# Performance work log

Measured on AMD Instinct MI355X. Metric: run time of the kernel, lower is better.

## Reference

```python
import jax, jax.numpy as jnp
import numpy as np

B, N, D_MODEL, H, D_FF, NB_FEAT = 2, 2048, 512, 8, 2048, 256
DH = D_MODEL // H


def layer_norm(x, g, b, eps=1e-5):
    mu = jnp.mean(x, axis=-1, keepdims=True)
    var = jnp.mean((x - mu) ** 2, axis=-1, keepdims=True)
    return g * (x - mu) / jnp.sqrt(var + eps) + b


def softmax_kernel(data, proj, is_query, eps=1e-4):
    # Performer FAVOR+ positive random features. data: [b,h,n,dh], proj: [m,dh]
    dn = data.shape[-1] ** -0.25
    ratio = proj.shape[0] ** -0.5
    dd = jnp.einsum('bhnd,jd->bhnj', dn * data, proj)
    diag = (jnp.sum(data ** 2, axis=-1, keepdims=True) * 0.5) * (dn ** 2)
    if is_query:
        m = jnp.max(dd, axis=-1, keepdims=True)
    else:
        m = jnp.max(dd)
    return ratio * (jnp.exp(dd - diag - m) + eps)


def setup_inputs() -> dict:
    key = jax.random.key(0)
    ks = jax.random.split(key, 12)
    sd = D_MODEL ** -0.5
    sf = D_FF ** -0.5
    return {
        'x': jax.random.normal(ks[0], (B, N, D_MODEL), jnp.float32),
        'Wq': jax.random.normal(ks[1], (D_MODEL, D_MODEL), jnp.float32) * sd,
        'bq': jnp.zeros((D_MODEL,), jnp.float32),
        'Wk': jax.random.normal(ks[2], (D_MODEL, D_MODEL), jnp.float32) * sd,
        'bk': jnp.zeros((D_MODEL,), jnp.float32),
        'Wv': jax.random.normal(ks[3], (D_MODEL, D_MODEL), jnp.float32) * sd,
        'bv': jnp.zeros((D_MODEL,), jnp.float32),
        'Wo': jax.random.normal(ks[4], (D_MODEL, D_MODEL), jnp.float32) * sd,
        'bo': jnp.zeros((D_MODEL,), jnp.float32),
        'proj': jax.random.normal(ks[5], (NB_FEAT, DH), jnp.float32),
        'W1': jax.random.normal(ks[6], (D_MODEL, D_FF), jnp.float32) * sd,
        'b1': jnp.zeros((D_FF,), jnp.float32),
        'W2': jax.random.normal(ks[7], (D_FF, D_MODEL), jnp.float32) * sf,
        'b2': jnp.zeros((D_MODEL,), jnp.float32),
        'g1': jnp.ones((D_MODEL,), jnp.float32),
        'beta1': jnp.zeros((D_MODEL,), jnp.float32),
        'g2': jnp.ones((D_MODEL,), jnp.float32),
        'beta2': jnp.zeros((D_MODEL,), jnp.float32),
    }


def reference(x, Wq, bq, Wk, bk, Wv, bv, Wo, bo, proj, W1, b1, W2, b2, g1, beta1, g2, beta2):
    b, n, d = x.shape
    heads = lambda W, bias: (x @ W + bias).reshape(b, n, H, DH).transpose(0, 2, 1, 3)  # bhnd
    q = softmax_kernel(heads(Wq, bq), proj, is_query=True)   # [b,h,n,m]
    k = softmax_kernel(heads(Wk, bk), proj, is_query=False)  # [b,h,n,m]
    v = heads(Wv, bv)                                        # [b,h,n,dh]
    # non-causal linear attention
    k_sum = jnp.sum(k, axis=-2)                                   # [b,h,m]
    D_inv = 1.0 / jnp.einsum('bhnf,bhf->bhn', q, k_sum)           # [b,h,n]
    context = jnp.einsum('bhnf,bhne->bhfe', k, v)                 # [b,h,m,dh]
    out = jnp.einsum('bhfe,bhnf,bhn->bhne', context, q, D_inv)    # [b,h,n,dh]
    # output_attentions=True: effective attention matrix (abs, head-mean, detached)
    attn = jnp.einsum('bhnf,bhmf->bhnm', q, k) * D_inv[..., None]
    attn_weight = jax.lax.stop_gradient(jnp.mean(jnp.abs(attn), axis=1))  # [b,n,n]
    out = out.transpose(0, 2, 1, 3).reshape(b, n, d)
    out = out @ Wo + bo
    # NOTE: original module has no residual connections
    h1 = layer_norm(out, g1, beta1)
    ff = jax.nn.relu(h1 @ W1 + b1) @ W2 + b2
    y = layer_norm(ff, g2, beta2)
    return y, attn_weight
```

## Files before the change

kernel.cpp:

```cpp
#include <hip/hip_runtime.h>
#include <math.h>

#define B_SZ   2
#define N_TOK  2048
#define DM     512
#define NH     8
#define DHH    64
#define NF     256
#define DFF    2048
#define HF     2048
#define LDQKV  1536

constexpr float DN_SCALE   = 0.35355339059327373f;
constexpr float DIAG_SCALE = 0.0625f;
constexpr float RATIO      = 0.0625f;
constexpr float FEPS       = 1e-4f;
constexpr float LN_EPS     = 1e-5f;

typedef __attribute__((ext_vector_type(8))) short bf16x8;
typedef __attribute__((ext_vector_type(8))) _Float16 f16x8;
typedef __attribute__((ext_vector_type(4))) float f32x4;

__device__ __forceinline__ short f2b(float f) {
  union { float f; unsigned u; } x; x.f = f;
  unsigned r = (x.u + 0x7fff + ((x.u >> 16) & 1)) >> 16;
  return (short)r;
}
__device__ __forceinline__ float b2f(short s) {
  union { unsigned u; float f; } x; x.u = ((unsigned)(unsigned short)s) << 16;
  return x.f;
}
__device__ __forceinline__ void gload16(const void* g, void* l) {
  __builtin_amdgcn_global_load_lds((const __attribute__((address_space(1))) void*)g,
                                   (__attribute__((address_space(3))) void*)l, 16, 0, 0);
}
__device__ __forceinline__ int swz64(int row, int kbyte) {
  return (row * 128 + kbyte) ^ ((row & 7) << 4);
}
__device__ __forceinline__ float reduce_bmax512(const float* __restrict__ bmax,
                                                float* __restrict__ red) {
  int t = threadIdx.x;
  float m = fmaxf(bmax[t], bmax[t + 256]);
  #pragma unroll
  for (int o = 1; o < 64; o <<= 1) m = fmaxf(m, __shfl_xor(m, o, 64));
  if ((t & 63) == 0) red[t >> 6] = m;
  __syncthreads();
  float r = fmaxf(fmaxf(red[0], red[1]), fmaxf(red[2], red[3]));
  __syncthreads();
  return r;
}

constexpr size_t OFF_CTXP  = 0;
constexpr size_t OFF_QB    = 4194304;
constexpr size_t OFF_OUT2  = 0;
constexpr size_t OFF_FF2   = 0;
constexpr size_t OFF_QFB   = 8388608;
constexpr size_t OFF_KB    = 12582912;
constexpr size_t OFF_QKV   = 16777216;
constexpr size_t OFF_FF1B  = 16777216;
constexpr size_t OFF_AOB   = 20971520;
constexpr size_t OFF_H1B   = 22020096;
constexpr size_t OFF_WOT   = 23068672;
constexpr size_t OFF_W1T   = 23199744;
constexpr size_t OFF_W2T   = 23724032;
constexpr size_t OFF_KSUM  = 24248320;
constexpr size_t OFF_DINV  = 24252416;
constexpr size_t OFF_CTXT  = 24285184;
constexpr size_t OFF_BMAX  = 24416256;
constexpr size_t OFF_ROWC  = 24416832;
constexpr size_t OFF_PART  = 24420928;
constexpr size_t OFF_VSUMP = 24552000;


template<bool RELU, bool OUT_BF16, bool BIAS>
__device__ __forceinline__ void gemm128_tile(short* As, short* Bs, int bx, int by,
                                             const short* __restrict__ A,
                                             const short* __restrict__ Bt,
                                             const float* __restrict__ bias,
                                             void* __restrict__ Cout, int K, int ldC) {
  int tid = threadIdx.x, lane = tid & 63, wave = tid >> 6;
  int wm = wave >> 1, wn = wave & 1;
  int bm = by * 128, bn = bx * 128;
  int srow = tid >> 3, scol = (tid & 7) * 8;
  f32x4 acc[4][4] = {};
  for (int k0 = 0; k0 < K; k0 += 64) {
    #pragma unroll
    for (int c = 0; c < 4; ++c) {
      int r = c * 32 + srow;
      gload16(A + (size_t)(bm + r) * K + k0 + scol, As + c * 2048 + wave * 512);
      gload16(Bt + (size_t)(bn + r) * K + k0 + scol, Bs + c * 2048 + wave * 512);
    }
    __syncthreads();
    #pragma unroll
    for (int kk = 0; kk < 2; ++kk) {
      bf16x8 af[4], bf[4];
      int kq = kk * 32 + (lane >> 4) * 8;
      #pragma unroll
      for (int i = 0; i < 4; ++i)
        af[i] = *(const bf16x8*)&As[(wm * 64 + i * 16 + (lane & 15)) * 64 + kq];
      #pragma unroll
      for (int j = 0; j < 4; ++j)
        bf[j] = *(const bf16x8*)&Bs[(wn * 64 + j * 16 + (lane & 15)) * 64 + kq];
      #pragma unroll
      for (int i = 0; i < 4; ++i)
        #pragma unroll
        for (int j = 0; j < 4; ++j)
          acc[i][j] = __builtin_amdgcn_mfma_f32_16x16x32_bf16(af[i], bf[j], acc[i][j], 0, 0, 0);
    }
    __syncthreads();
  }
  int row0 = bm + wm * 64, col0 = bn + wn * 64;
  #pragma unroll
  for (int i = 0; i < 4; ++i) {
    #pragma unroll
    for (int j = 0; j < 4; ++j) {
      int col = col0 + j * 16 + (lane & 15);
      float bv = BIAS ? bias[col] : 0.f;
      #pragma unroll
      for (int r = 0; r < 4; ++r) {
        int row = row0 + i * 16 + (lane >> 4) * 4 + r;
        float v = acc[i][j][r] + bv;
        if (RELU) v = fmaxf(v, 0.f);
        size_t off = (size_t)row * ldC + col;
        if (OUT_BF16) ((short*)Cout)[off] = f2b(v);
        else          ((float*)Cout)[off] = v;
      }
    }
  }
}

template<bool RELU, bool OUT_BF16>
__device__ __forceinline__ void bn64_tile(short* As, short* Bs, int bn, int bm,
                                          const short* __restrict__ A,
                                          const short* __restrict__ Bt,
                                          const float* __restrict__ bias,
                                          void* __restrict__ Cout, int N, int K) {
  int tid = threadIdx.x, lane = tid & 63, wave = tid >> 6;
  int srow = tid >> 3, scol = (tid & 7) * 8;
  f32x4 acc[2][4] = {};
  for (int k0 = 0; k0 < K; k0 += 64) {
    #pragma unroll
    for (int c = 0; c < 4; ++c)
      gload16(A + (size_t)(bm + c * 32 + srow) * K + k0 + scol, As + c * 2048 + wave * 512);
    #pragma unroll
    for (int c = 0; c < 2; ++c)
      gload16(Bt + (size_t)(bn + c * 32 + srow) * K + k0 + scol, Bs + c * 2048 + wave * 512);
    __syncthreads();
    #pragma unroll
    for (int kk = 0; kk < 2; ++kk) {
      bf16x8 af[2], bf[4];
      int kq = kk * 32 + (lane >> 4) * 8;
      #pragma unroll
      for (int i = 0; i < 2; ++i)
        af[i] = *(const bf16x8*)&As[(wave * 32 + i * 16 + (lane & 15)) * 64 + kq];
      #pragma unroll
      for (int j = 0; j < 4; ++j)
        bf[j] = *(const bf16x8*)&Bs[(j * 16 + (lane & 15)) * 64 + kq];
      #pragma unroll
      for (int i = 0; i < 2; ++i)
        #pragma unroll
        for (int j = 0; j < 4; ++j)
          acc[i][j] = __builtin_amdgcn_mfma_f32_16x16x32_bf16(af[i], bf[j], acc[i][j], 0, 0, 0);
    }
    __syncthreads();
  }
  #pragma unroll
  for (int i = 0; i < 2; ++i) {
    #pragma unroll
    for (int j = 0; j < 4; ++j) {
      int col = bn + j * 16 + (lane & 15);
      float bv = bias[col];
      #pragma unroll
      for (int r = 0; r < 4; ++r) {
        int row = bm + wave * 32 + i * 16 + (lane >> 4) * 4 + r;
        float v = acc[i][j][r] + bv;
        if (RELU) v = fmaxf(v, 0.f);
        if (OUT_BF16) ((short*)Cout)[(size_t)row * N + col] = f2b(v);
        else          ((float*)Cout)[(size_t)row * N + col] = v;
      }
    }
  }
}

__device__ __forceinline__ void pv_tile(short* As, short* Bs, int pid,
                                        const short* __restrict__ qfb,
                                        const short* __restrict__ ctxT,
                                        const float* __restrict__ Dinv,
                                        short* __restrict__ aob) {
  int tid = threadIdx.x, lane = tid & 63, wave = tid >> 6;
  int srow = tid >> 3, scol = (tid & 7) * 8;
  int bx = pid & 15, bh = pid >> 4;
  int b = bh >> 3, h = bh & 7;
  int n0 = bx * 128;

  f32x4 acc[2][4] = {};
  for (int k0 = 0; k0 < NF; k0 += 64) {
    #pragma unroll
    for (int c = 0; c < 4; ++c) {
      int r = c * 32 + srow;
      gload16(qfb + (size_t)(b * N_TOK + n0 + r) * HF + h * NF + k0 + scol,
              As + c * 2048 + wave * 512);
    }
    #pragma unroll
    for (int c = 0; c < 2; ++c) {
      int r = c * 32 + srow;
      gload16(ctxT + (size_t)bh * 16384 + (size_t)r * 256 + k0 + scol,
              Bs + c * 2048 + wave * 512);
    }
    __syncthreads();
    #pragma unroll
    for (int kk = 0; kk < 2; ++kk) {
      bf16x8 af[2], bf[4];
      int kq = kk * 32 + (lane >> 4) * 8;
      #pragma unroll
      for (int i = 0; i < 2; ++i)
        af[i] = *(const bf16x8*)&As[(wave * 32 + i * 16 + (lane & 15)) * 64 + kq];
      #pragma unroll
      for (int j = 0; j < 4; ++j)
        bf[j] = *(const bf16x8*)&Bs[(j * 16 + (lane & 15)) * 64 + kq];
      #pragma unroll
      for (int i = 0; i < 2; ++i)
        #pragma unroll
        for (int j = 0; j < 4; ++j)
          acc[i][j] = __builtin_amdgcn_mfma_f32_16x16x32_bf16(af[i], bf[j], acc[i][j], 0, 0, 0);
    }
    __syncthreads();
  }
  #pragma unroll
  for (int i = 0; i < 2; ++i) {
    #pragma unroll
    for (int j = 0; j < 4; ++j) {
      int e = j * 16 + (lane & 15);
      #pragma unroll
      for (int r = 0; r < 4; ++r) {
        int n = n0 + wave * 32 + i * 16 + (lane >> 4) * 4 + r;
        float dv = Dinv[bh * N_TOK + n];
        aob[(size_t)(b * N_TOK + n) * DM + h * DHH + e] = f2b(acc[i][j][r] * dv);
      }
    }
  }
}


__global__ __launch_bounds__(256)
void gemm_mfma_qkv(const short* __restrict__ A, const short* __restrict__ Bt,
                   float* __restrict__ Cout) {
  __shared__ short As[128 * 64];
  __shared__ short Bs[128 * 64];
  gemm128_tile<false, false, false>(As, Bs, blockIdx.x, blockIdx.y, A, Bt, nullptr,
                                    Cout, DM, LDQKV);
}

__global__ __launch_bounds__(256)
void pv_kernel(const short* __restrict__ qfb, const short* __restrict__ ctxT,
               const float* __restrict__ Dinv, short* __restrict__ aob) {
  __shared__ short As[128 * 64];
  __shared__ short Bs[64 * 64];
  pv_tile(As, Bs, blockIdx.x, qfb, ctxT, Dinv, aob);
}

__global__ __launch_bounds__(256)
void gemm_bn64_wo(const short* __restrict__ A, const short* __restrict__ Bt,
                  const float* __restrict__ bias, float* __restrict__ Cout) {
  __shared__ short As[128 * 64];
  __shared__ short Bs[64 * 64];
  bn64_tile<false, false>(As, Bs, blockIdx.x * 64, blockIdx.y * 128, A, Bt, bias, Cout, DM, DM);
}

template<bool RELU, bool OUT_BF16>
__global__ __launch_bounds__(256)
void gemm_bn64(const short* __restrict__ A, const short* __restrict__ Bt,
               const float* __restrict__ bias, void* __restrict__ Cout,
               int M, int N, int K) {
  __shared__ short As[128 * 64];
  __shared__ short Bs[64 * 64];
  bn64_tile<RELU, OUT_BF16>(As, Bs, blockIdx.x * 64, blockIdx.y * 128, A, Bt, bias, Cout, N, K);
}

__global__ __launch_bounds__(256)
void fatC1_kernel(const short* __restrict__ qb, const short* __restrict__ kb,
                  const float* __restrict__ rowc, float* __restrict__ attnw,
                  const short* __restrict__ h1b, const short* __restrict__ W1t,
                  const float* __restrict__ b1, short* __restrict__ ff1b) {
  __shared__ short As[2][128 * 64];
  __shared__ short Bs[2][128 * 64];
  int bid = blockIdx.x;
  int tid = threadIdx.x, lane = tid & 63, wave = tid >> 6;
  int srow = tid >> 3, scol = (tid & 7) * 8;

  if (bid < 512) {
    int z = bid >> 8, flat = bid & 255;
    int tile = flat >> 4, wi = flat & 15;
    int by = (tile >> 2) * 4 + (wi >> 2);
    int bx = (tile & 3) * 4 + (wi & 3);
    int bm = by * 128, bn = bx * 128;
    const short* Ab = qb + (size_t)z * N_TOK * HF;
    const short* Bb = kb + (size_t)z * N_TOK * HF;
    const float* rc = rowc + (size_t)z * N_TOK;
    float* out = attnw + (size_t)z * N_TOK * N_TOK;
    int wm = wave >> 1, wn = wave & 1;
    f32x4 acc[4][4] = {};

    #pragma unroll
    for (int c = 0; c < 4; ++c) {
      int r = c * 32 + srow;
      gload16(Ab + (size_t)(bm + r) * HF + scol, As[0] + c * 2048 + wave * 512);
      gload16(Bb + (size_t)(bn + r) * HF + scol, Bs[0] + c * 2048 + wave * 512);
    }
    for (int it = 0; it < HF / 64; ++it) {
      int cur = it & 1;
      if (it + 1 < HF / 64) {
        int k1 = (it + 1) * 64;
        short* An = As[cur ^ 1];
        short* Bn = Bs[cur ^ 1];
        #pragma unroll
        for (int c = 0; c < 4; ++c) {
          int r = c * 32 + srow;
          gload16(Ab + (size_t)(bm + r) * HF + k1 + scol, An + c * 2048 + wave * 512);
          gload16(Bb + (size_t)(bn + r) * HF + k1 + scol, Bn + c * 2048 + wave * 512);
        }
        asm volatile("s_waitcnt vmcnt(8)" ::: "memory");
      } else {
        asm volatile("s_waitcnt vmcnt(0)" ::: "memory");
      }
      __builtin_amdgcn_s_barrier();
      __builtin_amdgcn_sched_barrier(0);
      const short* Ac = As[cur];
      const short* Bc = Bs[cur];
      #pragma unroll
      for (int kk = 0; kk < 2; ++kk) {
        bf16x8 af[4], bf[4];
        int kq = kk * 32 + (lane >> 4) * 8;
        #pragma unroll
        for (int i = 0; i < 4; ++i)
          af[i] = *(const bf16x8*)&Ac[(wm * 64 + i * 16 + (lane & 15)) * 64 + kq];
        #pragma unroll
        for (int j = 0; j < 4; ++j)
          bf[j] = *(const bf16x8*)&Bc[(wn * 64 + j * 16 + (lane & 15)) * 64 + kq];
        #pragma unroll
        for (int i = 0; i < 4; ++i)
          #pragma unroll
          for (int j = 0; j < 4; ++j)
            acc[i][j] = __builtin_amdgcn_mfma_f32_16x16x32_bf16(af[i], bf[j], acc[i][j], 0, 0, 0);
      }
      __builtin_amdgcn_sched_barrier(0);
      __builtin_amdgcn_s_barrier();
    }
    int row0 = bm + wm * 64, col0 = bn + wn * 64;
    #pragma unroll
    for (int i = 0; i < 4; ++i) {
      #pragma unroll
      for (int j = 0; j < 4; ++j) {
        int col = col0 + j * 16 + (lane & 15);
        #pragma unroll
        for (int r = 0; r < 4; ++r) {
          int row = row0 + i * 16 + (lane >> 4) * 4 + r;
          out[(size_t)row * N_TOK + col] = acc[i][j][r] + rc[row];
        }
      }
    }
  } else {
    int flat = bid - 512;
    gemm128_tile<true, true, true>(As[0], Bs[0], flat & 15, flat >> 4, h1b, W1t, b1, ff1b,
                                   DM, DFF);
  }
}

__global__ void prep_kernel(const float* __restrict__ x, short* __restrict__ xb,
                            const float* Wq, const float* Wk, const float* Wv, const float* Wo,
                            short* Wqt, short* Wkt, short* Wvt, short* Wot,
                            const float* W1, short* W1t, const float* W2, short* W2t) {
  __shared__ float t[64][65];
  int id = blockIdx.x, tid = threadIdx.x;
  if (id >= 768) {
    size_t base = ((size_t)(id - 768) * 256 + tid) * 8;
    #pragma unroll
    for (int u = 0; u < 8; ++u) xb[base + u] = f2b(x[base + u]);
    return;
  }
  const float* W; short* Wt; int K, N, bx, by;
  if (id < 256) {
    int z = id >> 6, sub = id & 63;
    W  = (z == 0) ? Wq : (z == 1) ? Wk : (z == 2) ? Wv : Wo;
    Wt = (z == 0) ? Wqt : (z == 1) ? Wkt : (z == 2) ? Wvt : Wot;
    K = 512; N = 512; bx = sub & 7; by = sub >> 3;
  } else if (id < 512) {
    int sub = id - 256;
    W = W1; Wt = W1t; K = 512; N = 2048; bx = sub & 31; by = sub >> 5;
  } else {
    int sub = id - 512;
    W = W2; Wt = W2t; K = 2048; N = 512; bx = sub & 7; by = sub >> 3;
  }
  int k0 = by * 64, n0 = bx * 64;
  int lx = tid & 63, ly = tid >> 6;
  for (int r = ly; r < 64; r += 4)
    t[r][lx] = W[(size_t)(k0 + r) * N + n0 + lx];
  __syncthreads();
  for (int r = ly; r < 64; r += 4)
    Wt[(size_t)(n0 + r) * K + k0 + lx] = f2b(t[lx][r]);
}

__global__ __launch_bounds__(256)
void feat_mfma_kernel(const float* __restrict__ qkv, const float* __restrict__ bq,
                      const float* __restrict__ bk, const float* __restrict__ proj,
                      short* __restrict__ qfb, short* __restrict__ kbo,
                      float* __restrict__ part, float* __restrict__ bmax) {
  __shared__ short qh[64 * 64], ql[64 * 64];
  __shared__ short ph[128 * 64], pl[128 * 64];
  __shared__ float dpart[64][4];
  __shared__ float diag[64];
  __shared__ float wred[4];
  __shared__ float colp[4][256];
  int t = threadIdx.x;
  bool isq = (blockIdx.z == 0);
  int coff = isq ? 0 : 512;
  const float* bias = isq ? bq : bk;
  short* qout = isq ? qfb : kbo;
  int bh = blockIdx.y, b = bh >> 3, h = bh & 7;
  int n0 = blockIdx.x * 64;
  int lane = t & 63, w = t >> 6, l15 = lane & 15, lq = lane >> 4;

  {
    int r = t >> 2, cg = (t & 3) * 16;
    const float* src = qkv + (size_t)(b * N_TOK + n0 + r) * LDQKV + coff + h * 64 + cg;
    const float* bs = bias + h * 64 + cg;
    float ss = 0.f;
    #pragma unroll
    for (int c2 = 0; c2 < 2; ++c2) {
      f16x8 H, L;
      #pragma unroll
      for (int u = 0; u < 8; ++u) {
        float xv = src[c2 * 8 + u] + bs[c2 * 8 + u];
        ss += xv * xv;
        _Float16 hi = (_Float16)xv;
        H[u] = hi;
        L[u] = (_Float16)(xv - (float)hi);
      }
      int off = swz64(r, cg * 2 + c2 * 16);
      *(f16x8*)((char*)qh + off) = H;
      *(f16x8*)((char*)ql + off) = L;
    }
    dpart[r][t & 3] = ss;
  }
  __syncthreads();
  if (t < 64)
    diag[t] = (dpart[t][0] + dpart[t][1] + dpart[t][2] + dpart[t][3]) * DIAG_SCALE;

  f16x8 ah[2], al[2];
  #pragma unroll
  for (int kk = 0; kk < 2; ++kk) {
    int off = swz64(w * 16 + l15, kk * 64 + lq * 16);
    ah[kk] = *(f16x8*)((char*)qh + off);
    al[kk] = *(f16x8*)((char*)ql + off);
  }

  f32x4 acc[16] = {};
  #pragma unroll
  for (int half = 0; half < 2; ++half) {
    __syncthreads();
    {
      int r = t & 127, cg = (t >> 7) * 32;
      const float* src = proj + (size_t)(half * 128 + r) * DHH + cg;
      #pragma unroll
      for (int c2 = 0; c2 < 4; ++c2) {
        f16x8 H, L;
        #pragma unroll
        for (int u = 0; u < 8; ++u) {
          float xv = src[c2 * 8 + u];
          _Float16 hi = (_Float16)xv;
          H[u] = hi;
          L[u] = (_Float16)(xv - (float)hi);
        }
        int off = swz64(r, cg * 2 + c2 * 16);
        *(f16x8*)((char*)ph + off) = H;
        *(f16x8*)((char*)pl + off) = L;
      }
    }
    __syncthreads();
    #pragma unroll
    for (int jl = 0; jl < 8; ++jl) {
      int row = jl * 16 + l15;
      #pragma unroll
      for (int kk = 0; kk < 2; ++kk) {
        int off = swz64(row, kk * 64 + lq * 16);
        f16x8 bh8 = *(f16x8*)((char*)ph + off);
        f16x8 bl8 = *(f16x8*)((char*)pl + off);
        acc[half * 8 + jl] = __builtin_amdgcn_mfma_f32_16x16x32_f16(ah[kk], bh8, acc[half * 8 + jl], 0, 0, 0);
        acc[half * 8 + jl] = __builtin_amdgcn_mfma_f32_16x16x32_f16(al[kk], bh8, acc[half * 8 + jl], 0, 0, 0);
        acc[half * 8 + jl] = __builtin_amdgcn_mfma_f32_16x16x32_f16(ah[kk], bl8, acc[half * 8 + jl], 0, 0, 0);
      }
    }
  }

  if (isq) {
    #pragma unroll
    for (int r = 0; r < 4; ++r) {
      float mx = -3.4e38f;
      #pragma unroll
      for (int j = 0; j < 16; ++j) mx = fmaxf(mx, acc[j][r]);
      #pragma unroll
      for (int o = 1; o < 16; o <<= 1) mx = fmaxf(mx, __shfl_xor(mx, o, 64));
      int lrow = w * 16 + lq * 4 + r;
      float dg = diag[lrow];
      float ddm = mx * DN_SCALE;
      size_t base = (size_t)(b * N_TOK + n0 + lrow) * HF + h * NF + l15;
      #pragma unroll
      for (int j = 0; j < 16; ++j) {
        float v = RATIO * (expf(acc[j][r] * DN_SCALE - dg - ddm) + FEPS);
        qout[base + j * 16] = f2b(v);
      }
    }
  } else {
    float mxall = -3.4e38f;
    float cs[16];
    #pragma unroll
    for (int j = 0; j < 16; ++j) cs[j] = 0.f;
    #pragma unroll
    for (int r = 0; r < 4; ++r) {
      int lrow = w * 16 + lq * 4 + r;
      float dg = diag[lrow];
      size_t base = (size_t)(b * N_TOK + n0 + lrow) * HF + h * NF + l15;
      #pragma unroll
      for (int j = 0; j < 16; ++j) {
        float a = acc[j][r];
        mxall = fmaxf(mxall, a);
        float e = expf(a * DN_SCALE - dg);
        cs[j] += e;
        qout[base + j * 16] = f2b(e);
      }
    }
    #pragma unroll
    for (int j = 0; j < 16; ++j) {
      cs[j] += __shfl_xor(cs[j], 16, 64);
      cs[j] += __shfl_xor(cs[j], 32, 64);
    }
    if (lq == 0) {
      #pragma unroll
      for (int j = 0; j < 16; ++j) colp[w][j * 16 + l15] = cs[j];
    }
    #pragma unroll
    for (int o = 1; o < 64; o <<= 1) mxall = fmaxf(mxall, __shfl_xor(mxall, o, 64));
    if (lane == 0) wred[w] = mxall;
    __syncthreads();
    part[(size_t)(bh * 32 + blockIdx.x) * 256 + t] =
        colp[0][t] + colp[1][t] + colp[2][t] + colp[3][t];
    if (t == 0)
      bmax[bh * 32 + blockIdx.x] =
          fmaxf(fmaxf(wred[0], wred[1]), fmaxf(wred[2], wred[3])) * DN_SCALE;
  }
}

__global__ __launch_bounds__(256)
void ctx_part_kernel(const short* __restrict__ kb, const float* __restrict__ qkv,
                     const float* __restrict__ bv, float* __restrict__ ctxp,
                     float* __restrict__ vsump) {
  int bh = blockIdx.y, b = bh >> 3, h = bh & 7;
  int ns = blockIdx.z * 128;
  int tid = threadIdx.x;
  if (blockIdx.x == 4) {
    __shared__ float vred[4][64];
    int e = tid & 63, q = tid >> 6;
    float s = 0.f;
    for (int nn = q * 32; nn < q * 32 + 32; ++nn)
      s += qkv[(size_t)(b * N_TOK + ns + nn) * LDQKV + 1024 + h * DHH + e];
    vred[q][e] = s;
    __syncthreads();
    if (tid < 64)
      vsump[((size_t)blockIdx.z * 16 + bh) * 64 + tid] =
          vred[0][tid] + vred[1][tid] + vred[2][tid] + vred[3][tid] + 128.f * bv[h * DHH + tid];
    return;
  }
  int f0 = blockIdx.x * 64;
  __shared__ float kf[32][68];
  __shared__ float vs[32][68];
  int tf = (tid >> 4) * 4, te = (tid & 15) * 4;
  int nn8 = tid >> 3, f8 = (tid & 7) * 8;
  float bvv[8];
  #pragma unroll
  for (int u = 0; u < 8; ++u) bvv[u] = bv[h * DHH + f8 + u];
  float acc[4][4] = {};
  for (int n0 = ns; n0 < ns + 128; n0 += 32) {
    bf16x8 kv8 = *(const bf16x8*)&kb[(size_t)(b * N_TOK + n0 + nn8) * HF + h * NF + f0 + f8];
    #pragma unroll
    for (int u = 0; u < 8; ++u) kf[nn8][f8 + u] = b2f(kv8[u]);
    const float* vrow = qkv + (size_t)(b * N_TOK + n0 + nn8) * LDQKV + 1024 + h * DHH + f8;
    #pragma unroll
    for (int u = 0; u < 8; ++u) vs[nn8][f8 + u] = vrow[u] + bvv[u];
    __syncthreads();
    #pragma unroll
    for (int nn = 0; nn < 32; nn++) {
      float a[4], bb[4];
      #pragma unroll
      for (int i = 0; i < 4; i++) a[i] = kf[nn][tf + i];
      #pragma unroll
      for (int j = 0; j < 4; j++) bb[j] = vs[nn][te + j];
      #pragma unroll
      for (int i = 0; i < 4; i++)
        #pragma unroll
        for (int j = 0; j < 4; j++) acc[i][j] += a[i] * bb[j];
    }
    __syncthreads();
  }
  #pragma unroll
  for (int i = 0; i < 4; i++)
    #pragma unroll
    for (int j = 0; j < 4; j++)
      ctxp[(size_t)blockIdx.z * 262144 + (size_t)bh * 16384 +
           (size_t)(f0 + tf + i) * 64 + te + j] = acc[i][j];
}

__global__ __launch_bounds__(256)
void smallfat_kernel(const float* __restrict__ part, const float* __restrict__ bmax,
                     float* __restrict__ ksum, const float* __restrict__ ctxp,
                     const float* __restrict__ vsump, short* __restrict__ ctxT) {
  __shared__ float T[64][65];
  __shared__ float red[4];
  int t = threadIdx.x;
  float m = reduce_bmax512(bmax, red);
  float s = expf(-m);
  if (blockIdx.x < 16) {
    int bh = blockIdx.x;
    float sum = 0.f;
    #pragma unroll 8
    for (int c = 0; c < 32; ++c) sum += part[(size_t)(bh * 32 + c) * 256 + t];
    ksum[bh * 256 + t] = RATIO * (s * sum + (float)N_TOK * FEPS);
  } else {
    int id = blockIdx.x - 16;
    int ftile = id & 3, bh = id >> 2;
    int e = t & 63, q = t >> 6;
    float vsum_e = 0.f;
    #pragma unroll
    for (int c = 0; c < 16; ++c) vsum_e += vsump[((size_t)c * 16 + bh) * 64 + e];
    #pragma unroll
    for (int i = 0; i < 16; ++i) {
      int fl = i * 4 + q;
      size_t idx = (size_t)bh * 16384 + (size_t)(ftile * 64 + fl) * 64 + e;
      float sum = 0.f;
      #pragma unroll
      for (int c = 0; c < 16; ++c) sum += ctxp[(size_t)c * 262144 + idx];
      T[fl][e] = RATIO * (s * sum + FEPS * vsum_e);
    }
    __syncthreads();
    #pragma unroll
    for (int i = 0; i < 16; ++i) {
      int er = i * 4 + q;
      ctxT[(size_t)bh * 16384 + (size_t)er * 256 + ftile * 64 + e] = f2b(T[e][er]);
    }
  }
}

__global__ __launch_bounds__(256)
void dinvqs_kernel(const short* __restrict__ qfb, const float* __restrict__ ksum,
                   const float* __restrict__ bmax, float* __restrict__ Dinv,
                   float* __restrict__ rowc, short* __restrict__ qb) {
  __shared__ float red[4];
  __shared__ float wsum[4];
  int R = blockIdx.x;
  int b = R >> 11, n = R & 2047;
  int t = threadIdx.x;
  float m = reduce_bmax512(bmax, red);
  float sc = RATIO * expf(-m);
  bf16x8 qv = *(const bf16x8*)(qfb + (size_t)R * HF + t * 8);
  const float* ks = ksum + b * 2048 + t * 8;
  float p = 0.f;
  #pragma unroll
  for (int u = 0; u < 8; ++u) p += b2f(qv[u]) * ks[u];
  #pragma unroll
  for (int o = 1; o < 32; o <<= 1) p += __shfl_xor(p, o, 64);
  float d = 1.0f / p;
  if ((t & 31) == 0) Dinv[(b * NH + (t >> 5)) * N_TOK + n] = d;
  float dv = d * 0.125f;
  float qs = 0.f;
  bf16x8 o8;
  #pragma unroll
  for (int u = 0; u < 8; ++u) {
    float qb_f = b2f(qv[u]) * dv;
    qs += qb_f;
    o8[u] = f2b(qb_f * sc);
  }
  *(bf16x8*)(qb + (size_t)R * HF + t * 8) = o8;
  #pragma unroll
  for (int o = 1; o < 64; o <<= 1) qs += __shfl_xor(qs, o, 64);
  if ((t & 63) == 0) wsum[t >> 6] = qs;
  __syncthreads();
  if (t == 0) rowc[R] = RATIO * FEPS * (wsum[0] + wsum[1] + wsum[2] + wsum[3]);
}

template<bool OUT_BF16>
__global__ void ln_kernel(const float* __restrict__ x, const float* __restrict__ g,
                          const float* __restrict__ beta, void* __restrict__ y) {
  int row = blockIdx.x, t = threadIdx.x;
  __shared__ float red[4];
  __shared__ float bcast[2];
  const float* xr = x + (size_t)row * DM;
  float v0 = xr[t], v1 = xr[t + 256];
  float s = v0 + v1;
  #pragma unroll
  for (int o = 32; o > 0; o >>= 1) s += __shfl_xor(s, o, 64);
  if ((t & 63) == 0) red[t >> 6] = s;
  __syncthreads();
  if (t == 0) bcast[0] = (red[0] + red[1] + red[2] + red[3]) * (1.0f / 512.0f);
  __syncthreads();
  float mean = bcast[0];
  float d0 = v0 - mean, d1 = v1 - mean;
  float s2 = d0 * d0 + d1 * d1;
  #pragma unroll
  for (int o = 32; o > 0; o >>= 1) s2 += __shfl_xor(s2, o, 64);
  if ((t & 63) == 0) red[t >> 6] = s2;
  __syncthreads();
  if (t == 0) bcast[1] = (red[0] + red[1] + red[2] + red[3]) * (1.0f / 512.0f);
  __syncthreads();
  float inv = rsqrtf(bcast[1] + LN_EPS);
  float o0 = g[t] * d0 * inv + beta[t];
  float o1 = g[t + 256] * d1 * inv + beta[t + 256];
  if (OUT_BF16) {
    ((short*)y)[(size_t)row * DM + t] = f2b(o0);
    ((short*)y)[(size_t)row * DM + t + 256] = f2b(o1);
  } else {
    ((float*)y)[(size_t)row * DM + t] = o0;
    ((float*)y)[(size_t)row * DM + t + 256] = o1;
  }
}

extern "C" void kernel_launch(void* const* d_in, const int* in_sizes, int n_in,
                              void* d_out, int out_size, void* d_ws, size_t ws_size,
                              hipStream_t stream) {
  const float* x     = (const float*)d_in[0];
  const float* Wq    = (const float*)d_in[1];
  const float* bq    = (const float*)d_in[2];
  const float* Wk    = (const float*)d_in[3];
  const float* bk    = (const float*)d_in[4];
  const float* Wv    = (const float*)d_in[5];
  const float* bv    = (const float*)d_in[6];
  const float* Wo    = (const float*)d_in[7];
  const float* bo    = (const float*)d_in[8];
  const float* proj  = (const float*)d_in[9];
  const float* W1    = (const float*)d_in[10];
  const float* b1    = (const float*)d_in[11];
  const float* W2    = (const float*)d_in[12];
  const float* b2    = (const float*)d_in[13];
  const float* g1    = (const float*)d_in[14];
  const float* beta1 = (const float*)d_in[15];
  const float* g2    = (const float*)d_in[16];
  const float* beta2 = (const float*)d_in[17];

  float* ws = (float*)d_ws;
  float* y_out = (float*)d_out;
  float* attnw = y_out + (size_t)B_SZ * N_TOK * DM;

  float* ctxp  = ws + OFF_CTXP;
  short* qb    = (short*)(ws + OFF_QB);
  float* out2  = ws + OFF_OUT2;
  float* ff2   = ws + OFF_FF2;
  short* ff1b  = (short*)(ws + OFF_FF1B);
  short* qfb   = (short*)(ws + OFF_QFB);
  short* xb    = (short*)(ws + OFF_QFB);
  short* kb    = (short*)(ws + OFF_KB);
  short* Wqkvt = (short*)(ws + OFF_KB);
  float* QKVlin = ws + OFF_QKV;
  short* aob   = (short*)(ws + OFF_AOB);
  short* h1b   = (short*)(ws + OFF_H1B);
  short* Wot   = (short*)(ws + OFF_WOT);
  short* W1t   = (short*)(ws + OFF_W1T);
  short* W2t   = (short*)(ws + OFF_W2T);
  float* ksum  = ws + OFF_KSUM;
  float* Dinv  = ws + OFF_DINV;
  short* ctxT  = (short*)(ws + OFF_CTXT);
  float* bmax  = ws + OFF_BMAX;
  float* rowc  = ws + OFF_ROWC;
  float* part  = ws + OFF_PART;
  float* vsump = ws + OFF_VSUMP;

  dim3 blk(256);
  int MT = B_SZ * N_TOK;

  prep_kernel<<<1792, blk, 0, stream>>>(x, xb, Wq, Wk, Wv, Wo,
                                        Wqkvt, Wqkvt + 262144, Wqkvt + 524288, Wot,
                                        W1, W1t, W2, W2t);

  gemm_mfma_qkv<<<dim3(LDQKV / 128, MT / 128), blk, 0, stream>>>(xb, Wqkvt, QKVlin);

  feat_mfma_kernel<<<dim3(N_TOK / 64, B_SZ * NH, 2), blk, 0, stream>>>(
      QKVlin, bq, bk, proj, qfb, kb, part, bmax);

  ctx_part_kernel<<<dim3(5, B_SZ * NH, 16), blk, 0, stream>>>(kb, QKVlin, bv, ctxp, vsump);

  smallfat_kernel<<<80, blk, 0, stream>>>(part, bmax, ksum, ctxp, vsump, ctxT);

  dinvqs_kernel<<<MT, blk, 0, stream>>>(qfb, ksum, bmax, Dinv, rowc, qb);

  pv_kernel<<<dim3(N_TOK / 128 * B_SZ * NH), blk, 0, stream>>>(qfb, ctxT, Dinv, aob);

  gemm_bn64_wo<<<dim3(DM / 64, MT / 128), blk, 0, stream>>>(aob, Wot, bo, out2);

  ln_kernel<true><<<MT, blk, 0, stream>>>(out2, g1, beta1, h1b);

  fatC1_kernel<<<1024, blk, 0, stream>>>(qb, kb, rowc, attnw, h1b, W1t, b1, ff1b);

  gemm_bn64<false, false><<<dim3(DM / 64, MT / 128), blk, 0, stream>>>(
      ff1b, W2t, b2, ff2, MT, DM, DFF);

  ln_kernel<false><<<MT, blk, 0, stream>>>(ff2, g2, beta2, y_out);
}
```

Before: 224.0 us.

## Use 256x128 tiles with 8-wave blocks and distance-2 prefetch in fused attn/FF1 kernel

Replaces the 128x128, 4-wave fused attention-weight and FF1 GEMM kernel with 512-thread blocks computing 256x128 tiles. Each wave holds an 8x2 MFMA accumulator grid, and global-to-LDS loads are prefetched two K-steps ahead into a double buffer. Larger tiles raise arithmetic intensity and cut global traffic per flop, and the deeper prefetch is meant to hide load latency better. The trade-off is fewer blocks (512 instead of 1024), higher register and LDS use per block, and possible occupancy loss.

```diff
diff --git a/kernel.cpp b/kernel.cpp
--- a/kernel.cpp
+++ b/kernel.cpp
@@ -241,6 +241,93 @@
   }
 }
 
+__device__ __forceinline__ void stage_pipe(const short* __restrict__ Ag,
+                                           const short* __restrict__ Bg,
+                                           int bm, int bn, int k0, int K,
+                                           short* Al, short* Bl) {
+  int tid = threadIdx.x;
+  int sr = tid >> 3, sc = (tid & 7) * 8;
+  #pragma unroll
+  for (int c = 0; c < 4; ++c)
+    gload16(Ag + (size_t)(bm + c * 64 + sr) * K + k0 + sc, Al + (c * 64 + sr) * 64 + sc);
+  #pragma unroll
+  for (int c = 0; c < 2; ++c)
+    gload16(Bg + (size_t)(bn + c * 64 + sr) * K + k0 + sc, Bl + (c * 64 + sr) * 64 + sc);
+}
+
+template<int MODE>
+__device__ __forceinline__ void pipe_tile(short* As0, short* As1, short* Bs0, short* Bs1,
+                                          int bm, int bn,
+                                          const short* __restrict__ Ag,
+                                          const short* __restrict__ Bg,
+                                          const float* __restrict__ aux,
+                                          void* __restrict__ Cout, int K, int ldC) {
+  int tid = threadIdx.x, lane = tid & 63, wave = tid >> 6;
+  int wm = wave >> 2, wn = wave & 3;
+  int l15 = lane & 15, lq = lane >> 4;
+  int NT = K / 64;
+
+  f32x4 acc[8][2] = {};
+
+  stage_pipe(Ag, Bg, bm, bn, 0, K, As0, Bs0);
+  stage_pipe(Ag, Bg, bm, bn, 64, K, As1, Bs1);
+
+  for (int t = 0; t < NT; ++t) {
+    if (t + 1 < NT) asm volatile("s_waitcnt vmcnt(6)" ::: "memory");
+    else            asm volatile("s_waitcnt vmcnt(0)" ::: "memory");
+    __builtin_amdgcn_sched_barrier(0);
+    __builtin_amdgcn_s_barrier();
+    __builtin_amdgcn_sched_barrier(0);
+
+    const short* Ac = (t & 1) ? As1 : As0;
+    const short* Bc = (t & 1) ? Bs1 : Bs0;
+    #pragma unroll
+    for (int kk = 0; kk < 2; ++kk) {
+      int kq = kk * 32 + lq * 8;
+      bf16x8 af[8], bf[2];
+      #pragma unroll
+      for (int mi = 0; mi < 8; ++mi)
+        af[mi] = *(const bf16x8*)&Ac[(wm * 128 + mi * 16 + l15) * 64 + kq];
+      #pragma unroll
+      for (int nj = 0; nj < 2; ++nj)
+        bf[nj] = *(const bf16x8*)&Bc[(wn * 32 + nj * 16 + l15) * 64 + kq];
+      #pragma unroll
+      for (int mi = 0; mi < 8; ++mi)
+        #pragma unroll
+        for (int nj = 0; nj < 2; ++nj)
+          acc[mi][nj] = __builtin_amdgcn_mfma_f32_16x16x32_bf16(af[mi], bf[nj], acc[mi][nj], 0, 0, 0);
+    }
+    __builtin_amdgcn_sched_barrier(0);
+    __builtin_amdgcn_s_barrier();
+    __builtin_amdgcn_sched_barrier(0);
+
+    if (t + 2 < NT) {
+      short* An = (t & 1) ? As1 : As0;
+      short* Bn = (t & 1) ? Bs1 : Bs0;
+      stage_pipe(Ag, Bg, bm, bn, (t + 2) * 64, K, An, Bn);
+    }
+  }
+
+  #pragma unroll
+  for (int mi = 0; mi < 8; ++mi) {
+    #pragma unroll
+    for (int nj = 0; nj < 2; ++nj) {
+      int col = bn + wn * 32 + nj * 16 + l15;
+      float bv = (MODE == 1) ? aux[col] : 0.f;
+      #pragma unroll
+      for (int r = 0; r < 4; ++r) {
+        int row = bm + wm * 128 + mi * 16 + lq * 4 + r;
+        float v = acc[mi][nj][r];
+        if (MODE == 0) v += aux[row];
+        else           v = fmaxf(v + bv, 0.f);
+        size_t off = (size_t)row * ldC + col;
+        if (MODE == 0) ((float*)Cout)[off] = v;
+        else           ((short*)Cout)[off] = f2b(v);
+      }
+    }
+  }
+}
+
 
 __global__ __launch_bounds__(256)
 void gemm_mfma_qkv(const short* __restrict__ A, const short* __restrict__ Bt,
@@ -277,92 +364,26 @@
   bn64_tile<RELU, OUT_BF16>(As, Bs, blockIdx.x * 64, blockIdx.y * 128, A, Bt, bias, Cout, N, K);
 }
 
-__global__ __launch_bounds__(256)
-void fatC1_kernel(const short* __restrict__ qb, const short* __restrict__ kb,
-                  const float* __restrict__ rowc, float* __restrict__ attnw,
-                  const short* __restrict__ h1b, const short* __restrict__ W1t,
-                  const float* __restrict__ b1, short* __restrict__ ff1b) {
-  __shared__ short As[2][128 * 64];
+__global__ __launch_bounds__(512)
+void fat8_kernel(const short* __restrict__ qb, const short* __restrict__ kb,
+                 const float* __restrict__ rowc, float* __restrict__ attnw,
+                 const short* __restrict__ h1b, const short* __restrict__ W1t,
+                 const float* __restrict__ b1, short* __restrict__ ff1b) {
+  __shared__ short As[2][256 * 64];
   __shared__ short Bs[2][128 * 64];
   int bid = blockIdx.x;
-  int tid = threadIdx.x, lane = tid & 63, wave = tid >> 6;
-  int srow = tid >> 3, scol = (tid & 7) * 8;
-
-  if (bid < 512) {
-    int z = bid >> 8, flat = bid & 255;
-    int tile = flat >> 4, wi = flat & 15;
-    int by = (tile >> 2) * 4 + (wi >> 2);
-    int bx = (tile & 3) * 4 + (wi & 3);
-    int bm = by * 128, bn = bx * 128;
-    const short* Ab = qb + (size_t)z * N_TOK * HF;
-    const short* Bb = kb + (size_t)z * N_TOK * HF;
-    const float* rc = rowc + (size_t)z * N_TOK;
-    float* out = attnw + (size_t)z * N_TOK * N_TOK;
-    int wm = wave >> 1, wn = wave & 1;
-    f32x4 acc[4][4] = {};
-
-    #pragma unroll
-    for (int c = 0; c < 4; ++c) {
-      int r = c * 32 + srow;
-      gload16(Ab + (size_t)(bm + r) * HF + scol, As[0] + c * 2048 + wave * 512);
-      gload16(Bb + (size_t)(bn + r) * HF + scol, Bs[0] + c * 2048 + wave * 512);
-    }
-    for (int it = 0; it < HF / 64; ++it) {
-      int cur = it & 1;
-      if (it + 1 < HF / 64) {
-        int k1 = (it + 1) * 64;
-        short* An = As[cur ^ 1];
-        short* Bn = Bs[cur ^ 1];
-        #pragma unroll
-        for (int c = 0; c < 4; ++c) {
-          int r = c * 32 + srow;
-          gload16(Ab + (size_t)(bm + r) * HF + k1 + scol, An + c * 2048 + wave * 512);
-          gload16(Bb + (size_t)(bn + r) * HF + k1 + scol, Bn + c * 2048 + wave * 512);
-        }
-        asm volatile("s_waitcnt vmcnt(8)" ::: "memory");
-      } else {
-        asm volatile("s_waitcnt vmcnt(0)" ::: "memory");
-      }
-      __builtin_amdgcn_s_barrier();
-      __builtin_amdgcn_sched_barrier(0);
-      const short* Ac = As[cur];
-      const short* Bc = Bs[cur];
-      #pragma unroll
-      for (int kk = 0; kk < 2; ++kk) {
-        bf16x8 af[4], bf[4];
-        int kq = kk * 32 + (lane >> 4) * 8;
-        #pragma unroll
-        for (int i = 0; i < 4; ++i)
-          af[i] = *(const bf16x8*)&Ac[(wm * 64 + i * 16 + (lane & 15)) * 64 + kq];
-        #pragma unroll
-        for (int j = 0; j < 4; ++j)
-          bf[j] = *(const bf16x8*)&Bc[(wn * 64 + j * 16 + (lane & 15)) * 64 + kq];
-        #pragma unroll
-        for (int i = 0; i < 4; ++i)
-          #pragma unroll
-          for (int j = 0; j < 4; ++j)
-            acc[i][j] = __builtin_amdgcn_mfma_f32_16x16x32_bf16(af[i], bf[j], acc[i][j], 0, 0, 0);
-      }
-      __builtin_amdgcn_sched_barrier(0);
-      __builtin_amdgcn_s_barrier();
-    }
-    int row0 = bm + wm * 64, col0 = bn + wn * 64;
-    #pragma unroll
-    for (int i = 0; i < 4; ++i) {
-      #pragma unroll
-      for (int j = 0; j < 4; ++j) {
-        int col = col0 + j * 16 + (lane & 15);
-        #pragma unroll
-        for (int r = 0; r < 4; ++r) {
-          int row = row0 + i * 16 + (lane >> 4) * 4 + r;
-          out[(size_t)row * N_TOK + col] = acc[i][j][r] + rc[row];
-        }
-      }
-    }
+  if (bid < 256) {
+    int z = bid >> 7, tile = bid & 127;
+    int by = tile >> 4, bx = tile & 15;
+    pipe_tile<0>(As[0], As[1], Bs[0], Bs[1], by * 256, bx * 128,
+                 qb + (size_t)z * N_TOK * HF, kb + (size_t)z * N_TOK * HF,
+                 rowc + (size_t)z * N_TOK,
+                 attnw + (size_t)z * N_TOK * N_TOK, HF, N_TOK);
   } else {
-    int flat = bid - 512;
-    gemm128_tile<true, true, true>(As[0], Bs[0], flat & 15, flat >> 4, h1b, W1t, b1, ff1b,
-                                   DM, DFF);
+    int tile = bid - 256;
+    int by = tile >> 4, bx = tile & 15;
+    pipe_tile<1>(As[0], As[1], Bs[0], Bs[1], by * 256, bx * 128,
+                 h1b, W1t, b1, ff1b, DM, DFF);
   }
 }
 
@@ -795,7 +816,7 @@
 
   ln_kernel<true><<<MT, blk, 0, stream>>>(out2, g1, beta1, h1b);
 
-  fatC1_kernel<<<1024, blk, 0, stream>>>(qb, kb, rowc, attnw, h1b, W1t, b1, ff1b);
+  fat8_kernel<<<512, dim3(512), 0, stream>>>(qb, kb, rowc, attnw, h1b, W1t, b1, ff1b);
 
   gemm_bn64<false, false><<<dim3(DM / 64, MT / 128), blk, 0, stream>>>(
       ff1b, W2t, b2, ff2, MT, DM, DFF);
```

Result: slower. 243.8 us (+8.8%).
